# Optimization experiments

Hardware: AMD Instinct MI355X
Metric: run time of the kernel (lower is better)

## Reference

```python
import jax, jax.numpy as jnp
import numpy as np

B, Q, C, H, W, E, HID_ATT, HID_MLP, NUM_CLASSES, NUM_LABELS = 8, 64, 512, 16, 16, 512, 128, 512, 14, 64


def setup_inputs() -> dict:
    key = jax.random.key(0)
    ks = jax.random.split(key, 16)
    s = 0.02
    return {
        "feature": jax.random.normal(ks[0], (B, C, H, W), jnp.float32),
        "label_ids": jax.random.randint(ks[1], (B, Q), 0, NUM_LABELS),
        "query_table": jax.random.normal(ks[2], (NUM_LABELS, E), jnp.float32) * s,
        "W_film": jax.random.normal(ks[3], (E, 2 * C), jnp.float32) * s,
        "b_film": jnp.zeros((2 * C,), jnp.float32),
        "W_att_h": jax.random.normal(ks[4], (C, HID_ATT), jnp.float32) * s,
        "b_att_h": jnp.zeros((HID_ATT,), jnp.float32),
        "W_att_f": jax.random.normal(ks[5], (HID_ATT, 1), jnp.float32) * s,
        "b_att_f": jnp.zeros((1,), jnp.float32),
        "W_mlp1": jax.random.normal(ks[6], (C, HID_MLP), jnp.float32) * s,
        "b_mlp1": jnp.zeros((HID_MLP,), jnp.float32),
        "W_mlp2": jax.random.normal(ks[7], (HID_MLP, NUM_CLASSES), jnp.float32) * s,
        "b_mlp2": jnp.zeros((NUM_CLASSES,), jnp.float32),
    }


def gelu(x):
    return jax.nn.gelu(x, approximate=False)  # torch default GELU is exact erf


def reference(feature, label_ids, query_table, W_film, b_film, W_att_h, b_att_h,
              W_att_f, b_att_f, W_mlp1, b_mlp1, W_mlp2, b_mlp2):
    # query embedding lookup: (B, Q, E)
    qe = query_table[label_ids]
    # flatten spatial: (B, HW, C)
    f = feature.reshape(feature.shape[0], feature.shape[1], -1).transpose(0, 2, 1)
    # FiLM params from queries: (B, Q, 2C) -> gamma, beta (B, Q, C)
    gb = jnp.einsum("bqe,ec->bqc", qe, W_film) + b_film
    gamma, beta = jnp.split(gb, 2, axis=-1)
    # FiLM-modulated features: (B, Q, HW, C)
    film = f[:, None, :, :] * gamma[:, :, None, :] + beta[:, :, None, :]
    # local attention MLP -> sigmoid gate (B, Q, HW, 1)
    hidden = gelu(jnp.einsum("bqnc,ch->bqnh", film, W_att_h) + b_att_h)
    attn = jax.nn.sigmoid(jnp.einsum("bqnh,ho->bqno", hidden, W_att_f) + b_att_f)
    # weighted sum pool over HW, normalized by attention mass
    pooled = (attn * film).sum(axis=2) / (attn.sum(axis=2) + 1e-8)  # (B, Q, C)
    # classification MLP
    logits = jnp.einsum("bqh,ho->bqo", gelu(jnp.einsum("bqc,ch->bqh", pooled, W_mlp1) + b_mlp1), W_mlp2) + b_mlp2
    return logits  # (B, Q, NUM_CLASSES)
```

## Files before the change

### kernel.cpp

```cpp
#include <hip/hip_runtime.h>
#include <hip/hip_bf16.h>

#define B_    8
#define Q_    64
#define C_    512
#define HW_   256
#define E_    512
#define HATT_ 128
#define HMLP_ 512
#define NCLS_ 14
#define NLAB_ 64

typedef unsigned short u16;
typedef unsigned int   u32;
typedef __attribute__((ext_vector_type(8))) short short8;
typedef __attribute__((ext_vector_type(4))) float f32x4;


__device__ __forceinline__ float gelu_fast(float x) {
    const float ax = fabsf(x);
    const float t  = __builtin_amdgcn_rcpf(1.0f + 0.3275911f * ax);
    const float p  = t * (0.254829592f +
                     t * (-0.284496736f +
                     t * (1.421413741f +
                     t * (-1.453152027f +
                     t * 1.061405429f))));
    const float e  = __expf(-x * x);
    const float er = copysignf(1.0f - p * e, x);
    return 0.5f * x * (1.0f + er);
}
__device__ __forceinline__ float sigmoid_(float x) {
    return 1.0f / (1.0f + __expf(-x));
}
__device__ __forceinline__ u16 f2bf(float x) {
    u32 u = __float_as_uint(x);
    u32 r = (u + 0x7fffu + ((u >> 16) & 1u)) >> 16;
    return (u16)r;
}
__device__ __forceinline__ float bf2f(u16 u) {
    return __uint_as_float(((u32)u) << 16);
}
__device__ __forceinline__ void gl2lds16(const void* gsrc, void* ldsdst) {
    __builtin_amdgcn_global_load_lds(
        (const __attribute__((address_space(1))) u32*)gsrc,
        (__attribute__((address_space(3))) u32*)ldsdst, 16, 0, 0);
}

__global__ __launch_bounds__(256) void prep_gbp(
    const float* __restrict__ qt, const float* __restrict__ W_film,
    float* __restrict__ GBp) {
    __shared__ float qrow[128];
    const int bid = blockIdx.x, t = threadIdx.x;
    const int l = bid >> 2, cq = bid & 3;
    if (t < 128) qrow[t] = qt[l * E_ + cq * 128 + t];
    __syncthreads();
    const float* wp = W_film + (size_t)(cq * 128) * 1024 + t * 4;
    f32x4 a = {0.f, 0.f, 0.f, 0.f};
    #pragma unroll 8
    for (int c = 0; c < 128; ++c) {
        const float4 w = *(const float4*)(wp + (size_t)c * 1024);
        const float q = qrow[c];
        a.x += q * w.x; a.y += q * w.y; a.z += q * w.z; a.w += q * w.w;
    }
    *(f32x4*)&GBp[(size_t)bid * 1024 + t * 4] = a;
}

__global__ __launch_bounds__(256) void prep_rest(
    const float* __restrict__ feature, const float* __restrict__ W_mlp1,
    const int* __restrict__ label_ids, const float* __restrict__ b_film,
    const float* __restrict__ W_att_h, const float* __restrict__ GBp,
    u16* __restrict__ W1bf, u16* __restrict__ fT, int* __restrict__ perm,
    float* __restrict__ Gl, float* __restrict__ Bl,
    u16* __restrict__ WgT, float* __restrict__ Dlp) {

    __shared__ __align__(16) char sm[16896];
    const int bid = blockIdx.x, t = threadIdx.x;

    if (bid < 256) {
        float (*tile)[65] = (float(*)[65])sm;
        const int b = bid >> 5, c0 = ((bid >> 2) & 7) * 64, n0 = (bid & 3) * 64;
        const float* fb = feature + (size_t)b * C_ * HW_;
        const int cl = t >> 2, nq = t & 3;
        #pragma unroll
        for (int i = 0; i < 4; ++i) {
            float4 v = *(const float4*)&fb[(c0 + cl) * HW_ + n0 + nq * 16 + i * 4];
            tile[cl][nq * 16 + i * 4 + 0] = v.x;
            tile[cl][nq * 16 + i * 4 + 1] = v.y;
            tile[cl][nq * 16 + i * 4 + 2] = v.z;
            tile[cl][nq * 16 + i * 4 + 3] = v.w;
        }
        __syncthreads();
        const int nl = t >> 2, cqq = t & 3;
        u16 pk[16];
        #pragma unroll
        for (int k = 0; k < 16; ++k) pk[k] = f2bf(tile[cqq * 16 + k][nl]);
        u16* dst = fT + (size_t)(b * HW_ + n0 + nl) * C_ + c0 + cqq * 16;
        *(uint4*)dst       = *(uint4*)pk;
        *(uint4*)(dst + 8) = *(uint4*)(pk + 8);
    } else if (bid < 320) {
        const int b2 = bid - 256;
        #pragma unroll
        for (int k = 0; k < 2; ++k) {
            const int idx = (b2 * 512 + k * 256 + t) * 8;
            float4 v0 = *(const float4*)&W_mlp1[idx];
            float4 v1 = *(const float4*)&W_mlp1[idx + 4];
            u16 pk[8] = {f2bf(v0.x), f2bf(v0.y), f2bf(v0.z), f2bf(v0.w),
                         f2bf(v1.x), f2bf(v1.y), f2bf(v1.z), f2bf(v1.w)};
            *(uint4*)&W1bf[idx] = *(uint4*)pk;
        }
    } else if (bid == 320) {
        int* cnt = (int*)sm;
        if (t < 64) cnt[t] = 0;
        __syncthreads();
        const int l0 = label_ids[t], l1 = label_ids[t + 256];
        atomicAdd(&cnt[l0], 1);
        atomicAdd(&cnt[l1], 1);
        __syncthreads();
        if (t == 0) {
            int run = 0;
            for (int i = 0; i < 64; ++i) { const int c = cnt[i]; cnt[i] = run; run += c; }
        }
        __syncthreads();
        const int p0 = atomicAdd(&cnt[l0], 1);
        perm[p0] = t | (l0 << 16);
        const int p1 = atomicAdd(&cnt[l1], 1);
        perm[p1] = (t + 256) | (l1 << 16);
    } else {
        float* g_s  = (float*)sm;
        float* b_s  = g_s + 128;
        float* dred = b_s + 128;
        const int wb = bid - 321;
        const int l = wb >> 2, cq = wb & 3;

        if (t < 128) {
            const int c = cq * 128 + t;
            float g = b_film[c], be = b_film[512 + c];
            #pragma unroll
            for (int j = 0; j < 4; ++j) {
                g  += GBp[(size_t)(l * 4 + j) * 1024 + c];
                be += GBp[(size_t)(l * 4 + j) * 1024 + 512 + c];
            }
            g_s[t] = g; b_s[t] = be;
            Gl[l * C_ + c] = g;
            Bl[l * C_ + c] = be;
        }
        __syncthreads();

        const int h = t & 127, ch = t >> 7;
        const int hswz = (h >> 1) & 3;
        float dl = 0.f;
        #pragma unroll
        for (int sl = 0; sl < 2; ++sl) {
            const int ss = cq * 4 + ch * 2 + sl;
            char* dst = (char*)WgT + (size_t)l * 131072 + ss * 8192 + h * 64;
            #pragma unroll
            for (int g = 0; g < 4; ++g) {
                u16 pk[8];
                #pragma unroll
                for (int j = 0; j < 8; ++j) {
                    const int cl = ch * 64 + sl * 32 + g * 8 + j;
                    const float w = W_att_h[(size_t)(cq * 128 + cl) * HATT_ + h];
                    pk[j] = f2bf(g_s[cl] * w);
                    dl += b_s[cl] * w;
                }
                *(uint4*)(dst + ((g ^ hswz) * 16)) = *(uint4*)pk;
            }
        }
        dred[t] = dl;
        __syncthreads();
        if (t < 128)
            Dlp[(size_t)(l * 4 + cq) * 128 + t] = dred[t] + dred[128 + t];
    }
}

__global__ __launch_bounds__(256, 4) void attn_gemm(
    const float* __restrict__ W_att_f, const float* __restrict__ b_att_f,
    const float* __restrict__ b_att_h, const float* __restrict__ Dlp,
    const int*   __restrict__ perm,    const u16* __restrict__ WgT,
    const u16*   __restrict__ fT,
    u16* __restrict__ pPb, float* __restrict__ pA) {

    __shared__ __align__(16) char Ash[2][8192];
    __shared__ __align__(16) char Bsh[2][8192];
    __shared__ float d_s[HATT_];
    __shared__ float wf_s[HATT_];
    __shared__ float attn_part[2][128];
    __shared__ float attn_s[128];

    const int t = threadIdx.x;
    const int idx = blockIdx.x;
    const int srank2 = (idx & 7) * 128 + (idx >> 3);
    const int r = srank2 >> 1, nh = srank2 & 1;
    const int pe = perm[r];
    const int bq = pe & 0xffff, l = pe >> 16;
    const int b = bq >> 6;

    if (t < HATT_) {
        d_s[t] = b_att_h[t]
               + Dlp[(size_t)(l * 4 + 0) * 128 + t]
               + Dlp[(size_t)(l * 4 + 1) * 128 + t]
               + Dlp[(size_t)(l * 4 + 2) * 128 + t]
               + Dlp[(size_t)(l * 4 + 3) * 128 + t];
        wf_s[t] = W_att_f[t];
    }

    const u16* fTb = fT + (size_t)b * HW_ * C_ + (size_t)nh * 128 * C_;
    const u16* Wl  = WgT + (size_t)l * 65536;

    const int an0  = t >> 2;
    const int asl0 = (t & 3) ^ ((an0 >> 1) & 3);

    #define STAGE(s_) {                                                       \
        _Pragma("unroll")                                                     \
        for (int it = 0; it < 2; ++it)                                        \
            gl2lds16(fTb + (size_t)(it * 64 + an0) * C_ + (s_) * 32           \
                         + asl0 * 8,                                          \
                     &Ash[(s_) & 1][(it * 256 + t) * 16]);                    \
        _Pragma("unroll")                                                     \
        for (int it = 0; it < 2; ++it)                                        \
            gl2lds16(Wl + (size_t)(s_) * 4096 + (size_t)(it * 256 + t) * 8,   \
                     &Bsh[(s_) & 1][(it * 256 + t) * 16]);                    \
    }

    const int lane = t & 63, w = t >> 6;
    const int wm = w >> 1, wc = w & 1;
    const int lr = lane & 15, lk = lane >> 4;

    const f32x4 zero = {0.f, 0.f, 0.f, 0.f};
    f32x4 acc[4][4];
    #pragma unroll
    for (int mi = 0; mi < 4; ++mi)
        #pragma unroll
        for (int ni = 0; ni < 4; ++ni) acc[mi][ni] = zero;

    STAGE(0);
    __syncthreads();

    #pragma unroll 2
    for (int s = 0; s < 16; ++s) {
        if (s < 15) STAGE(s + 1);
        const char* Ab = Ash[s & 1];
        const char* Bb = Bsh[s & 1];
        short8 af[4], bf[4];
        #pragma unroll
        for (int mi = 0; mi < 4; ++mi) {
            const int nl = wm * 64 + mi * 16 + lr;
            af[mi] = *(const short8*)(Ab + nl * 64 + ((lk ^ ((nl >> 1) & 3)) * 16));
        }
        #pragma unroll
        for (int ni = 0; ni < 4; ++ni) {
            const int h = wc * 64 + ni * 16 + lr;
            bf[ni] = *(const short8*)(Bb + h * 64 + ((lk ^ ((h >> 1) & 3)) * 16));
        }
        #pragma unroll
        for (int mi = 0; mi < 4; ++mi)
            #pragma unroll
            for (int ni = 0; ni < 4; ++ni)
                acc[mi][ni] = __builtin_amdgcn_mfma_f32_16x16x32_bf16(
                    af[mi], bf[ni], acc[mi][ni], 0, 0, 0);
        __syncthreads();
    }

    #pragma unroll
    for (int mi = 0; mi < 4; ++mi) {
        #pragma unroll
        for (int j = 0; j < 4; ++j) {
            float sum = 0.f;
            #pragma unroll
            for (int ni = 0; ni < 4; ++ni) {
                const int h = wc * 64 + ni * 16 + lr;
                sum += gelu_fast(acc[mi][ni][j] + d_s[h]) * wf_s[h];
            }
            sum += __shfl_xor(sum, 1);
            sum += __shfl_xor(sum, 2);
            sum += __shfl_xor(sum, 4);
            sum += __shfl_xor(sum, 8);
            if (lr == 0) attn_part[wc][wm * 64 + mi * 16 + lk * 4 + j] = sum;
        }
    }
    __syncthreads();
    if (t < 128)
        attn_s[t] = sigmoid_(attn_part[0][t] + attn_part[1][t] + b_att_f[0]);
    __syncthreads();
    if (t < 64) {
        float a = attn_s[t] + attn_s[t + 64];
        #pragma unroll
        for (int m = 1; m < 64; m <<= 1) a += __shfl_xor(a, m);
        if (t == 0) pA[bq * 2 + nh] = a;
    }

    float* pred = (float*)Ash;
    {
        const int ng = t >> 7, cb = (t & 127) * 4;
        const u16* fp = fTb + cb;
        f32x4 p = zero;
        #pragma unroll 8
        for (int n = ng * 64; n < ng * 64 + 64; ++n) {
            const uint2 v = *(const uint2*)(fp + (size_t)n * C_);
            const float a = attn_s[n];
            p.x += a * __uint_as_float(v.x << 16);
            p.y += a * __uint_as_float(v.x & 0xffff0000u);
            p.z += a * __uint_as_float(v.y << 16);
            p.w += a * __uint_as_float(v.y & 0xffff0000u);
        }
        *(f32x4*)&pred[ng * 512 + cb] = p;
    }
    __syncthreads();
    {
        const int c0 = t * 2;
        const float v0 = pred[c0]     + pred[512 + c0];
        const float v1 = pred[c0 + 1] + pred[512 + c0 + 1];
        u16 pk[2] = {f2bf(v0), f2bf(v1)};
        *(u32*)&pPb[(size_t)(bq * 2 + nh) * 512 + c0] = *(u32*)pk;
    }
}

__global__ __launch_bounds__(512) void mlp_head(
    const int*   __restrict__ label_ids,
    const float* __restrict__ Gl, const float* __restrict__ Bl,
    const float* __restrict__ b_mlp1, const float* __restrict__ W_mlp2,
    const float* __restrict__ b_mlp2, const u16* __restrict__ pPb,
    const float* __restrict__ pA,     const u16* __restrict__ W1bf,
    float* __restrict__ out) {

    __shared__ float pooled_s[2][C_];
    __shared__ float zred[2][2][HMLP_];
    __shared__ float z_s[2][HMLP_];
    __shared__ float red_s[32 * NCLS_];

    const int t = threadIdx.x;
    const int bq0 = blockIdx.x * 2;

    {
        const int bqi = t >> 8, cc = (t & 255) * 2;
        const int bq = bq0 + bqi, l = label_ids[bq];
        const float A = pA[bq * 2] + pA[bq * 2 + 1];
        const float inv = 1.0f / (A + 1e-8f);
        #pragma unroll
        for (int i = 0; i < 2; ++i) {
            const int c = cc + i;
            const float p = bf2f(pPb[(size_t)(bq * 2) * 512 + c])
                          + bf2f(pPb[(size_t)(bq * 2 + 1) * 512 + c]);
            pooled_s[bqi][c] = (Gl[l * C_ + c] * p + Bl[l * C_ + c] * A) * inv;
        }
    }
    __syncthreads();

    {
        const int hp = t & 255, cg = t >> 8;
        float z00 = 0.f, z01 = 0.f, z10 = 0.f, z11 = 0.f;
        const u16* wp = W1bf + hp * 2;
        #pragma unroll 8
        for (int c = cg * 256; c < cg * 256 + 256; ++c) {
            const u32 v = *(const u32*)(wp + (size_t)c * HMLP_);
            const float w0 = __uint_as_float(v << 16);
            const float w1 = __uint_as_float(v & 0xffff0000u);
            const float pa = pooled_s[0][c], pb = pooled_s[1][c];
            z00 += pa * w0; z01 += pa * w1;
            z10 += pb * w0; z11 += pb * w1;
        }
        float2 a0 = {z00, z01}, a1 = {z10, z11};
        *(float2*)&zred[cg][0][hp * 2] = a0;
        *(float2*)&zred[cg][1][hp * 2] = a1;
    }
    __syncthreads();
    {
        const int bqi = t >> 8, h2 = (t & 255) * 2;
        #pragma unroll
        for (int i = 0; i < 2; ++i) {
            const int h = h2 + i;
            z_s[bqi][h] = gelu_fast(zred[0][bqi][h] + zred[1][bqi][h] + b_mlp1[h]);
        }
    }
    __syncthreads();

    #pragma unroll
    for (int bqi = 0; bqi < 2; ++bqi) {
        if (t < 448) {
            const int o = t % 14, seg = t / 14;
            float s = 0.f;
            #pragma unroll
            for (int k = 0; k < 16; ++k) {
                const int h = seg * 16 + k;
                s += z_s[bqi][h] * W_mlp2[h * NCLS_ + o];
            }
            red_s[seg * NCLS_ + o] = s;
        }
        __syncthreads();
        if (t < NCLS_) {
            float s = b_mlp2[t];
            #pragma unroll
            for (int seg = 0; seg < 32; ++seg) s += red_s[seg * NCLS_ + t];
            out[(bq0 + bqi) * NCLS_ + t] = s;
        }
        __syncthreads();
    }
}

extern "C" void kernel_launch(void* const* d_in, const int* in_sizes, int n_in,
                              void* d_out, int out_size, void* d_ws, size_t ws_size,
                              hipStream_t stream) {
    const float* feature   = (const float*)d_in[0];
    const int*   label_ids = (const int*)  d_in[1];
    const float* qt        = (const float*)d_in[2];
    const float* W_film    = (const float*)d_in[3];
    const float* b_film    = (const float*)d_in[4];
    const float* W_att_h   = (const float*)d_in[5];
    const float* b_att_h   = (const float*)d_in[6];
    const float* W_att_f   = (const float*)d_in[7];
    const float* b_att_f   = (const float*)d_in[8];
    const float* W_mlp1    = (const float*)d_in[9];
    const float* b_mlp1    = (const float*)d_in[10];
    const float* W_mlp2    = (const float*)d_in[11];
    const float* b_mlp2    = (const float*)d_in[12];
    float* out = (float*)d_out;

    char* wsb   = (char*)d_ws;
    float* GBp  = (float*)wsb;
    u16*   pPb  = (u16*)  wsb;
    float* pA   = (float*)(wsb + 1048576);
    int*   perm = (int*)  (wsb + 1052672);
    float* Dlp  = (float*)(wsb + 1054720);
    float* Gl   = (float*)(wsb + 1185792);
    float* Bl   = (float*)(wsb + 1316864);
    u16*   W1bf = (u16*)  (wsb + 1447936);
    u16*   fTp  = (u16*)  (wsb + 1972224);
    u16*   WgT  = (u16*)  (wsb + 4069376);

    hipLaunchKernelGGL(prep_gbp, dim3(256), dim3(256), 0, stream,
                       qt, W_film, GBp);
    hipLaunchKernelGGL(prep_rest, dim3(577), dim3(256), 0, stream,
                       feature, W_mlp1, label_ids, b_film, W_att_h, GBp,
                       W1bf, fTp, perm, Gl, Bl, WgT, Dlp);
    hipLaunchKernelGGL(attn_gemm, dim3(1024), dim3(256), 0, stream,
                       W_att_f, b_att_f, b_att_h, Dlp, perm, WgT, fTp, pPb, pA);
    hipLaunchKernelGGL(mlp_head, dim3(256), dim3(512), 0, stream,
                       label_ids, Gl, Bl, b_mlp1, W_mlp2, b_mlp2,
                       pPb, pA, W1bf, out);
}
```

Before: 68.50 us.

## Split pooling into MFMA pool_gemm, deepen attn pipeline, fuse FiLM reduction

Several changes land together. The FiLM gamma/beta projection now runs as a single full-K kernel with the bias folded in, which removes the partial-sum buffer and its later reduction, and Dl is accumulated with atomics after a memset. The attn_gemm main loop moves to a three-stage prefetch with explicit vmcnt waits and barriers. The per-block scalar weighted pooling over HW is removed: attention weights are written out in bf16 and a new pool_gemm kernel computes the pooled sums per batch with MFMA, reading the fp32 features directly. The cost is an extra kernel launch plus a memset, and slightly lower precision because attention is rounded to bf16.

```diff
diff --git a/kernel.cpp b/kernel.cpp
--- a/kernel.cpp
+++ b/kernel.cpp
@@ -40,38 +40,54 @@
 __device__ __forceinline__ float bf2f(u16 u) {
     return __uint_as_float(((u32)u) << 16);
 }
+__device__ __forceinline__ u32 cvt_pk_bf16(float lo, float hi) {
+    u32 r;
+    asm("v_cvt_pk_bf16_f32 %0, %1, %2" : "=v"(r) : "v"(lo), "v"(hi));
+    return r;
+}
 __device__ __forceinline__ void gl2lds16(const void* gsrc, void* ldsdst) {
     __builtin_amdgcn_global_load_lds(
         (const __attribute__((address_space(1))) u32*)gsrc,
         (__attribute__((address_space(3))) u32*)ldsdst, 16, 0, 0);
 }
 
-__global__ __launch_bounds__(256) void prep_gbp(
+__global__ __launch_bounds__(256) void prep_gbp2(
     const float* __restrict__ qt, const float* __restrict__ W_film,
-    float* __restrict__ GBp) {
-    __shared__ float qrow[128];
+    const float* __restrict__ b_film,
+    float* __restrict__ Gf, float* __restrict__ Bf) {
+    __shared__ float q_s[8][512];
     const int bid = blockIdx.x, t = threadIdx.x;
-    const int l = bid >> 2, cq = bid & 3;
-    if (t < 128) qrow[t] = qt[l * E_ + cq * 128 + t];
-    __syncthreads();
-    const float* wp = W_film + (size_t)(cq * 128) * 1024 + t * 4;
-    f32x4 a = {0.f, 0.f, 0.f, 0.f};
+    const int lg = bid >> 3, js = bid & 7, j0 = js * 128;
+
+    const float4* qsrc = (const float4*)(qt + (size_t)lg * 8 * 512);
+    #pragma unroll
+    for (int k = 0; k < 4; ++k)
+        ((float4*)q_s)[k * 256 + t] = qsrc[k * 256 + t];
+    __syncthreads();
+
+    const int tl = t >> 5, jq = t & 31;
+    const int j = j0 + jq * 4;
+    f32x4 a;
+    { const float4 bv = *(const float4*)&b_film[j];
+      a.x = bv.x; a.y = bv.y; a.z = bv.z; a.w = bv.w; }
+    const float* wp = W_film + j;
     #pragma unroll 8
-    for (int c = 0; c < 128; ++c) {
+    for (int c = 0; c < 512; ++c) {
         const float4 w = *(const float4*)(wp + (size_t)c * 1024);
-        const float q = qrow[c];
+        const float q = q_s[tl][c];
         a.x += q * w.x; a.y += q * w.y; a.z += q * w.z; a.w += q * w.w;
     }
-    *(f32x4*)&GBp[(size_t)bid * 1024 + t * 4] = a;
+    const int l = lg * 8 + tl;
+    if (j < 512) *(f32x4*)&Gf[(size_t)l * 512 + j] = a;
+    else         *(f32x4*)&Bf[(size_t)l * 512 + j - 512] = a;
 }
 
 __global__ __launch_bounds__(256) void prep_rest(
     const float* __restrict__ feature, const float* __restrict__ W_mlp1,
-    const int* __restrict__ label_ids, const float* __restrict__ b_film,
-    const float* __restrict__ W_att_h, const float* __restrict__ GBp,
+    const int* __restrict__ label_ids, const float* __restrict__ W_att_h,
+    const float* __restrict__ Gf, const float* __restrict__ Bf,
     u16* __restrict__ W1bf, u16* __restrict__ fT, int* __restrict__ perm,
-    float* __restrict__ Gl, float* __restrict__ Bl,
-    u16* __restrict__ WgT, float* __restrict__ Dlp) {
+    u16* __restrict__ WgT, float* __restrict__ Dl) {
 
     __shared__ __align__(16) char sm[16896];
     const int bid = blockIdx.x, t = threadIdx.x;
@@ -134,15 +150,8 @@
 
         if (t < 128) {
             const int c = cq * 128 + t;
-            float g = b_film[c], be = b_film[512 + c];
-            #pragma unroll
-            for (int j = 0; j < 4; ++j) {
-                g  += GBp[(size_t)(l * 4 + j) * 1024 + c];
-                be += GBp[(size_t)(l * 4 + j) * 1024 + 512 + c];
-            }
-            g_s[t] = g; b_s[t] = be;
-            Gl[l * C_ + c] = g;
-            Bl[l * C_ + c] = be;
+            g_s[t] = Gf[(size_t)l * 512 + c];
+            b_s[t] = Bf[(size_t)l * 512 + c];
         }
         __syncthreads();
 
@@ -169,16 +178,16 @@
         dred[t] = dl;
         __syncthreads();
         if (t < 128)
-            Dlp[(size_t)(l * 4 + cq) * 128 + t] = dred[t] + dred[128 + t];
+            atomicAdd(&Dl[(size_t)l * 128 + t], dred[t] + dred[128 + t]);
     }
 }
 
 __global__ __launch_bounds__(256, 4) void attn_gemm(
     const float* __restrict__ W_att_f, const float* __restrict__ b_att_f,
-    const float* __restrict__ b_att_h, const float* __restrict__ Dlp,
+    const float* __restrict__ b_att_h, const float* __restrict__ Dl,
     const int*   __restrict__ perm,    const u16* __restrict__ WgT,
     const u16*   __restrict__ fT,
-    u16* __restrict__ pPb, float* __restrict__ pA) {
+    u16* __restrict__ attA, float* __restrict__ pA) {
 
     __shared__ __align__(16) char Ash[2][8192];
     __shared__ __align__(16) char Bsh[2][8192];
@@ -196,11 +205,7 @@
     const int b = bq >> 6;
 
     if (t < HATT_) {
-        d_s[t] = b_att_h[t]
-               + Dlp[(size_t)(l * 4 + 0) * 128 + t]
-               + Dlp[(size_t)(l * 4 + 1) * 128 + t]
-               + Dlp[(size_t)(l * 4 + 2) * 128 + t]
-               + Dlp[(size_t)(l * 4 + 3) * 128 + t];
+        d_s[t]  = b_att_h[t] + Dl[(size_t)l * 128 + t];
         wf_s[t] = W_att_f[t];
     }
 
@@ -234,11 +239,13 @@
         for (int ni = 0; ni < 4; ++ni) acc[mi][ni] = zero;
 
     STAGE(0);
-    __syncthreads();
-
-    #pragma unroll 2
+    STAGE(1);
+    asm volatile("s_waitcnt vmcnt(4)" ::: "memory");
+    __builtin_amdgcn_sched_barrier(0);
+    __builtin_amdgcn_s_barrier();
+
+    #pragma unroll
     for (int s = 0; s < 16; ++s) {
-        if (s < 15) STAGE(s + 1);
         const char* Ab = Ash[s & 1];
         const char* Bb = Bsh[s & 1];
         short8 af[4], bf[4];
@@ -252,13 +259,23 @@
             const int h = wc * 64 + ni * 16 + lr;
             bf[ni] = *(const short8*)(Bb + h * 64 + ((lk ^ ((h >> 1) & 3)) * 16));
         }
+        asm volatile("s_waitcnt lgkmcnt(0)" ::: "memory");
+        __builtin_amdgcn_sched_barrier(0);
+        __builtin_amdgcn_s_barrier();
+        if (s < 14) STAGE(s + 2);
         #pragma unroll
         for (int mi = 0; mi < 4; ++mi)
             #pragma unroll
             for (int ni = 0; ni < 4; ++ni)
                 acc[mi][ni] = __builtin_amdgcn_mfma_f32_16x16x32_bf16(
                     af[mi], bf[ni], acc[mi][ni], 0, 0, 0);
-        __syncthreads();
+        if (s < 15) {
+            __builtin_amdgcn_sched_barrier(0);
+            if (s < 14) asm volatile("s_waitcnt vmcnt(4)" ::: "memory");
+            else        asm volatile("s_waitcnt vmcnt(0)" ::: "memory");
+            __builtin_amdgcn_sched_barrier(0);
+            __builtin_amdgcn_s_barrier();
+        }
     }
 
     #pragma unroll
@@ -279,8 +296,11 @@
         }
     }
     __syncthreads();
-    if (t < 128)
-        attn_s[t] = sigmoid_(attn_part[0][t] + attn_part[1][t] + b_att_f[0]);
+    if (t < 128) {
+        const u16 ab = f2bf(sigmoid_(attn_part[0][t] + attn_part[1][t] + b_att_f[0]));
+        attA[(size_t)bq * 256 + nh * 128 + t] = ab;
+        attn_s[t] = bf2f(ab);
+    }
     __syncthreads();
     if (t < 64) {
         float a = attn_s[t] + attn_s[t + 64];
@@ -288,38 +308,56 @@
         for (int m = 1; m < 64; m <<= 1) a += __shfl_xor(a, m);
         if (t == 0) pA[bq * 2 + nh] = a;
     }
-
-    float* pred = (float*)Ash;
-    {
-        const int ng = t >> 7, cb = (t & 127) * 4;
-        const u16* fp = fTb + cb;
-        f32x4 p = zero;
-        #pragma unroll 8
-        for (int n = ng * 64; n < ng * 64 + 64; ++n) {
-            const uint2 v = *(const uint2*)(fp + (size_t)n * C_);
-            const float a = attn_s[n];
-            p.x += a * __uint_as_float(v.x << 16);
-            p.y += a * __uint_as_float(v.x & 0xffff0000u);
-            p.z += a * __uint_as_float(v.y << 16);
-            p.w += a * __uint_as_float(v.y & 0xffff0000u);
-        }
-        *(f32x4*)&pred[ng * 512 + cb] = p;
-    }
-    __syncthreads();
-    {
-        const int c0 = t * 2;
-        const float v0 = pred[c0]     + pred[512 + c0];
-        const float v1 = pred[c0 + 1] + pred[512 + c0 + 1];
-        u16 pk[2] = {f2bf(v0), f2bf(v1)};
-        *(u32*)&pPb[(size_t)(bq * 2 + nh) * 512 + c0] = *(u32*)pk;
-    }
+}
+
+__global__ __launch_bounds__(256) void pool_gemm(
+    const float* __restrict__ feature, const u16* __restrict__ attA,
+    u16* __restrict__ pPTb) {
+
+    const int t = threadIdx.x, bid = blockIdx.x;
+    const int b = bid >> 3, c0 = (bid & 7) * 64;
+    const int w = t >> 6, lane = t & 63;
+    const int lr = lane & 15, lk = lane >> 4;
+    const int crow = c0 + w * 16 + lr;
+
+    const float* fr = feature + ((size_t)b * C_ + crow) * HW_;
+    const u16*   ar = attA + (size_t)b * 64 * 256;
+
+    const f32x4 zero = {0.f, 0.f, 0.f, 0.f};
+    f32x4 acc[4];
+    #pragma unroll
+    for (int ni = 0; ni < 4; ++ni) acc[ni] = zero;
+
+    #pragma unroll
+    for (int ss = 0; ss < 8; ++ss) {
+        const int n0 = ss * 32 + lk * 8;
+        const float4 a0 = *(const float4*)&fr[n0];
+        const float4 a1 = *(const float4*)&fr[n0 + 4];
+        union { uint4 u; short8 s; } au;
+        au.u.x = cvt_pk_bf16(a0.x, a0.y);
+        au.u.y = cvt_pk_bf16(a0.z, a0.w);
+        au.u.z = cvt_pk_bf16(a1.x, a1.y);
+        au.u.w = cvt_pk_bf16(a1.z, a1.w);
+        #pragma unroll
+        for (int ni = 0; ni < 4; ++ni) {
+            const short8 bf = *(const short8*)(ar + (size_t)(ni * 16 + lr) * 256 + n0);
+            acc[ni] = __builtin_amdgcn_mfma_f32_16x16x32_bf16(au.s, bf, acc[ni], 0, 0, 0);
+        }
+    }
+    #pragma unroll
+    for (int ni = 0; ni < 4; ++ni)
+        #pragma unroll
+        for (int j = 0; j < 4; ++j) {
+            const int c = c0 + w * 16 + lk * 4 + j;
+            pPTb[((size_t)b * C_ + c) * 64 + ni * 16 + lr] = f2bf(acc[ni][j]);
+        }
 }
 
 __global__ __launch_bounds__(512) void mlp_head(
     const int*   __restrict__ label_ids,
-    const float* __restrict__ Gl, const float* __restrict__ Bl,
+    const float* __restrict__ Gf, const float* __restrict__ Bf,
     const float* __restrict__ b_mlp1, const float* __restrict__ W_mlp2,
-    const float* __restrict__ b_mlp2, const u16* __restrict__ pPb,
+    const float* __restrict__ b_mlp2, const u16* __restrict__ pPTb,
     const float* __restrict__ pA,     const u16* __restrict__ W1bf,
     float* __restrict__ out) {
 
@@ -334,14 +372,15 @@
     {
         const int bqi = t >> 8, cc = (t & 255) * 2;
         const int bq = bq0 + bqi, l = label_ids[bq];
+        const int b = bq >> 6, q = bq & 63;
         const float A = pA[bq * 2] + pA[bq * 2 + 1];
         const float inv = 1.0f / (A + 1e-8f);
         #pragma unroll
         for (int i = 0; i < 2; ++i) {
             const int c = cc + i;
-            const float p = bf2f(pPb[(size_t)(bq * 2) * 512 + c])
-                          + bf2f(pPb[(size_t)(bq * 2 + 1) * 512 + c]);
-            pooled_s[bqi][c] = (Gl[l * C_ + c] * p + Bl[l * C_ + c] * A) * inv;
+            const float p = bf2f(pPTb[((size_t)b * C_ + c) * 64 + q]);
+            pooled_s[bqi][c] = (Gf[(size_t)l * 512 + c] * p
+                              + Bf[(size_t)l * 512 + c] * A) * inv;
         }
     }
     __syncthreads();
@@ -416,25 +455,29 @@
     float* out = (float*)d_out;
 
     char* wsb   = (char*)d_ws;
-    float* GBp  = (float*)wsb;
-    u16*   pPb  = (u16*)  wsb;
-    float* pA   = (float*)(wsb + 1048576);
-    int*   perm = (int*)  (wsb + 1052672);
-    float* Dlp  = (float*)(wsb + 1054720);
-    float* Gl   = (float*)(wsb + 1185792);
-    float* Bl   = (float*)(wsb + 1316864);
-    u16*   W1bf = (u16*)  (wsb + 1447936);
-    u16*   fTp  = (u16*)  (wsb + 1972224);
-    u16*   WgT  = (u16*)  (wsb + 4069376);
-
-    hipLaunchKernelGGL(prep_gbp, dim3(256), dim3(256), 0, stream,
-                       qt, W_film, GBp);
+    u16*   pPTb = (u16*)  wsb;
+    float* pA   = (float*)(wsb + 524288);
+    int*   perm = (int*)  (wsb + 528384);
+    float* Dl   = (float*)(wsb + 530432);
+    float* Gf   = (float*)(wsb + 563200);
+    float* Bf   = (float*)(wsb + 694272);
+    u16*   W1bf = (u16*)  (wsb + 825344);
+    u16*   attA = (u16*)  (wsb + 1349632);
+    u16*   fTp  = (u16*)  (wsb + 1611776);
+    u16*   WgT  = (u16*)  (wsb + 3708928);
+
+    hipMemsetAsync(Dl, 0, 32768, stream);
+    hipLaunchKernelGGL(prep_gbp2, dim3(64), dim3(256), 0, stream,
+                       qt, W_film, b_film, Gf, Bf);
     hipLaunchKernelGGL(prep_rest, dim3(577), dim3(256), 0, stream,
-                       feature, W_mlp1, label_ids, b_film, W_att_h, GBp,
-                       W1bf, fTp, perm, Gl, Bl, WgT, Dlp);
+                       feature, W_mlp1, label_ids, W_att_h, Gf, Bf,
+                       W1bf, fTp, perm, WgT, Dl);
     hipLaunchKernelGGL(attn_gemm, dim3(1024), dim3(256), 0, stream,
-                       W_att_f, b_att_f, b_att_h, Dlp, perm, WgT, fTp, pPb, pA);
+                       W_att_f, b_att_f, b_att_h, Dl, perm, WgT, fTp,
+                       attA, pA);
+    hipLaunchKernelGGL(pool_gemm, dim3(64), dim3(256), 0, stream,
+                       feature, attA, pPTb);
     hipLaunchKernelGGL(mlp_head, dim3(256), dim3(512), 0, stream,
-                       label_ids, Gl, Bl, b_mlp1, W_mlp2, b_mlp2,
-                       pPb, pA, W1bf, out);
-}
+                       label_ids, Gf, Bf, b_mlp1, W_mlp2, b_mlp2,
+                       pPTb, pA, W1bf, out);
+}
```

Result: slower. 98.89 us (+44.4%).
